# Optimization experiments

Hardware: AMD Instinct MI355X
Metric: run time of the kernel (lower is better)

## Reference

```python
import jax, jax.numpy as jnp
import numpy as np

N, B, D, Q = 32, 36, 2048, 1024  # batch, objects, v_dim, q_dim


def setup_inputs() -> dict:
    key = jax.random.key(0)
    ks = jax.random.split(key, 6)
    sc = 0.02  # small init so ReLU chains stay well-scaled
    return {
        "v": jax.random.normal(ks[0], (N, B, D), jnp.float32),
        "q": jax.random.normal(ks[1], (N, Q), jnp.float32),
        "W1": jax.random.normal(ks[2], (D, D), jnp.float32) * sc,
        "b1": jnp.zeros((D,), jnp.float32),
        "W2": jax.random.normal(ks[3], (D, D), jnp.float32) * sc,
        "b2": jnp.zeros((D,), jnp.float32),
        "W3": jax.random.normal(ks[4], (Q, D), jnp.float32) * sc,
        "b3": jnp.zeros((D,), jnp.float32),
    }


def reference(v, q, W1, b1, W2, b2, W3, b3):
    # FCNet = ReLU(Linear(.)) with weight-norm folded, dropout=0 (eval).
    # Original calls linear3 twice (linear4 unused bug), so q_emb == q_emb2.
    qe = jax.nn.relu(q @ W3 + b3)  # (N, D)
    # pairs[n,i,j] = v[n,i]*qe[n] + v[n,j]*qe[n]  -> (N, B, B, D)
    pairs = (v[:, :, None, :] + v[:, None, :, :]) * qe[:, None, None, :]
    h = jax.nn.relu(jnp.einsum('nijd,de->nije', pairs, W1) + b1)  # linear1
    x = jnp.sum(h, axis=2)  # sum over j relations -> (N, B, D)
    return jax.nn.relu(x @ W2 + b2)  # linear2
```

## Files before the change

### kernel.cpp

```cpp
#include <hip/hip_runtime.h>
#include <stdint.h>

#define N_BATCH 32
#define B_OBJ   36
#define D_DIM   2048
#define Q_DIM   1024

typedef __bf16 bf16x8  __attribute__((ext_vector_type(8)));
typedef float  f32x4   __attribute__((ext_vector_type(4)));
typedef float  f32x16  __attribute__((ext_vector_type(16)));

__device__ __forceinline__ uint16_t f2bf(float f) {
    uint32_t u = __builtin_bit_cast(uint32_t, f);
    uint32_t r = (u + 0x7FFFu + ((u >> 16) & 1u)) >> 16;
    return (uint16_t)r;
}

__device__ __forceinline__ void gld_lds16(const void* g, void* l) {
    __builtin_amdgcn_global_load_lds(
        (const __attribute__((address_space(1))) uint32_t*)g,
        (__attribute__((address_space(3))) uint32_t*)l, 16, 0, 0);
}

__global__ __launch_bounds__(256) void transpose_all(
    const float* __restrict__ W1, const float* __restrict__ W2,
    uint16_t* __restrict__ W1t, uint16_t* __restrict__ W2t) {
    __shared__ float tile[64][65];
    int gy = blockIdx.y;
    const float* W; uint16_t* Wt; int k0;
    if (gy < 32) { W = W1; Wt = W1t; k0 = gy * 64; }
    else         { W = W2; Wt = W2t; k0 = (gy - 32) * 64; }
    int n0 = blockIdx.x * 64;
    int t = threadIdx.x;
    {
        int r = t >> 4, c = (t & 15) * 4;
#pragma unroll
        for (int p = 0; p < 4; ++p)
            *(float4*)&tile[r + p * 16][c] =
                *(const float4*)&W[(size_t)(k0 + r + p * 16) * 2048 + n0 + c];
    }
    __syncthreads();
    {
        int n = t >> 2, kb = (t & 3) * 16;
#pragma unroll
        for (int g4 = 0; g4 < 4; ++g4) {
            int k = kb + g4 * 4;
            ushort4 o;
            o.x = f2bf(tile[k][n]);     o.y = f2bf(tile[k + 1][n]);
            o.z = f2bf(tile[k + 2][n]); o.w = f2bf(tile[k + 3][n]);
            *(ushort4*)&Wt[(size_t)(n0 + n) * 2048 + k0 + k] = o;
        }
    }
}

__global__ __launch_bounds__(256) void qe_f32(
    const float* __restrict__ q, const float* __restrict__ W3,
    float* __restrict__ qpart) {
    __shared__ float qs[128][32];
    int t = threadIdx.x;
    int e0 = blockIdx.x * 64;
    int kbase = blockIdx.y * 128;
    {
        int nn = t >> 3, kg = (t & 7) * 16;
#pragma unroll
        for (int p = 0; p < 4; ++p) {
            float4 f = *(const float4*)&q[(size_t)nn * Q_DIM + kbase + kg + p * 4];
            qs[kg + p * 4 + 0][nn] = f.x; qs[kg + p * 4 + 1][nn] = f.y;
            qs[kg + p * 4 + 2][nn] = f.z; qs[kg + p * 4 + 3][nn] = f.w;
        }
    }
    __syncthreads();
    int n = t >> 3, e8 = (t & 7) * 8;
    float acc[8] = {};
#pragma unroll 4
    for (int k = 0; k < 128; ++k) {
        float qv = qs[k][n];
        float4 wa = *(const float4*)&W3[(size_t)(kbase + k) * D_DIM + e0 + e8];
        float4 wb = *(const float4*)&W3[(size_t)(kbase + k) * D_DIM + e0 + e8 + 4];
        acc[0] += qv * wa.x; acc[1] += qv * wa.y; acc[2] += qv * wa.z; acc[3] += qv * wa.w;
        acc[4] += qv * wb.x; acc[5] += qv * wb.y; acc[6] += qv * wb.z; acc[7] += qv * wb.w;
    }
    float* dst = qpart + (size_t)blockIdx.y * 32 * D_DIM + (size_t)n * D_DIM + e0 + e8;
    *(float4*)dst = *(float4*)&acc[0];
    *(float4*)(dst + 4) = *(float4*)&acc[4];
}

__global__ __launch_bounds__(256) void qe_makeu(
    const float* __restrict__ qpart, const float* __restrict__ b3,
    const float* __restrict__ v, uint16_t* __restrict__ u) {
    int n = blockIdx.y;
    int c4 = blockIdx.x * 256 + threadIdx.x;
    const float4* p = (const float4*)qpart;
    size_t base = (size_t)n * 512 + c4;
    float4 s = p[base];
#pragma unroll
    for (int z = 1; z < 8; ++z) {
        float4 sz = p[(size_t)z * 16384 + base];
        s.x += sz.x; s.y += sz.y; s.z += sz.z; s.w += sz.w;
    }
    float4 b = ((const float4*)b3)[c4];
    float4 qe;
    qe.x = fmaxf(s.x + b.x, 0.f); qe.y = fmaxf(s.y + b.y, 0.f);
    qe.z = fmaxf(s.z + b.z, 0.f); qe.w = fmaxf(s.w + b.w, 0.f);
    const float4* v4 = (const float4*)v + (size_t)n * B_OBJ * 512 + c4;
    ushort4* u4 = (ushort4*)u + (size_t)n * B_OBJ * 512 + c4;
#pragma unroll 4
    for (int i = 0; i < B_OBJ; ++i) {
        float4 vv = v4[(size_t)i * 512];
        ushort4 o;
        o.x = f2bf(vv.x * qe.x); o.y = f2bf(vv.y * qe.y);
        o.z = f2bf(vv.z * qe.z); o.w = f2bf(vv.w * qe.w);
        u4[(size_t)i * 512] = o;
    }
}

__global__ __launch_bounds__(128) void gemm_fused(
    const uint16_t* __restrict__ A,
    const uint16_t* __restrict__ Bt,
    const float* __restrict__ bias,
    void* __restrict__ Cv,
    int mode) {
    __shared__ __align__(16) uint16_t sm[20480];
    float* yt = (float*)sm;

    int t = threadIdx.x, lane = t & 63, wave = t >> 6;
    int l31 = lane & 31, khalf = lane >> 5;
    int bg = blockIdx.y;
    int n0 = blockIdx.x * 64;
    const uint16_t* Ab = A + (size_t)bg * 72 * D_DIM;

    const uint16_t* gp[10]; uint16_t* lp[10]; int bufstep[10];
    {
        int row16 = lane >> 2, kin = (lane & 3) * 8;
#pragma unroll
        for (int c = 0; c < 10; ++c) {
            int r = wave * 10 + c;
            if (r < 12) {
                int h = r / 6, g = r % 6;
                gp[c] = Ab + (size_t)(g * 16 + row16) * D_DIM + h * 32 + kin;
                lp[c] = sm + h * 3072 + g * 512;
                bufstep[c] = 6144;
            } else {
                int rb = r - 12, h = rb >> 2, g = rb & 3;
                gp[c] = Bt + (size_t)(n0 + g * 16 + row16) * D_DIM + h * 32 + kin;
                lp[c] = sm + 12288 + h * 2048 + g * 512;
                bufstep[c] = 4096;
            }
        }
    }

    f32x16 acc[3] = {};

#pragma unroll
    for (int c = 0; c < 10; ++c) gld_lds16(gp[c], lp[c]);

    for (int it = 0; it < 32; ++it) {
        int buf = it & 1;
        __syncthreads();
        if (it < 31) {
            int nxt = buf ^ 1;
#pragma unroll
            for (int c = 0; c < 10; ++c)
                gld_lds16(gp[c] + (size_t)(it + 1) * 64, lp[c] + nxt * bufstep[c]);
        }
#pragma unroll
        for (int s = 0; s < 4; ++s) {
            int h = s >> 1, kin = (s & 1) * 16 + khalf * 8;
            bf16x8 bfr = *(const bf16x8*)(sm + 12288 + buf * 4096 + h * 2048 +
                                          (wave * 32 + l31) * 32 + kin);
#pragma unroll
            for (int mt = 0; mt < 3; ++mt) {
                bf16x8 af = *(const bf16x8*)(sm + buf * 6144 + h * 3072 +
                                             (mt * 32 + l31) * 32 + kin);
                acc[mt] = __builtin_amdgcn_mfma_f32_32x32x16_bf16(af, bfr, acc[mt], 0, 0, 0);
            }
        }
    }

    if (mode == 0) {
        uint16_t* X = (uint16_t*)Cv;
        __syncthreads();
#pragma unroll
        for (int mt = 0; mt < 3; ++mt)
#pragma unroll
            for (int reg = 0; reg < 16; ++reg) {
                int row = mt * 32 + (reg & 3) + 8 * (reg >> 2) + 4 * khalf;
                if (row < 72) yt[row * 68 + wave * 32 + l31] = acc[mt][reg];
            }
        __syncthreads();
        int col = t & 63, half = t >> 6;
        float b = bias[n0 + col];
        float z[36];
#pragma unroll
        for (int j = 0; j < 36; ++j) z[j] = yt[(half * 36 + j) * 68 + col];
        uint16_t* xb = X + (size_t)(bg * 72 + half * 36) * D_DIM + n0 + col;
#pragma unroll
        for (int i = 0; i < 36; ++i) {
            float zi = z[i] + b;
            float ssum = 0.f;
#pragma unroll
            for (int j = 0; j < 36; ++j) ssum += fmaxf(zi + z[j], 0.f);
            xb[(size_t)i * D_DIM] = f2bf(ssum);
        }
    } else {
        float* O = (float*)Cv;
        int col = n0 + wave * 32 + l31;
        float b = bias[col];
#pragma unroll
        for (int mt = 0; mt < 3; ++mt)
#pragma unroll
            for (int reg = 0; reg < 16; ++reg) {
                int row = mt * 32 + (reg & 3) + 8 * (reg >> 2) + 4 * khalf;
                if (row < 72)
                    O[(size_t)(bg * 72 + row) * D_DIM + col] =
                        fmaxf(acc[mt][reg] + b, 0.f);
            }
    }
}

extern "C" void kernel_launch(void* const* d_in, const int* in_sizes, int n_in,
                              void* d_out, int out_size, void* d_ws, size_t ws_size,
                              hipStream_t stream) {
    const float* v  = (const float*)d_in[0];
    const float* q  = (const float*)d_in[1];
    const float* W1 = (const float*)d_in[2];
    const float* b1 = (const float*)d_in[3];
    const float* W2 = (const float*)d_in[4];
    const float* b2 = (const float*)d_in[5];
    const float* W3 = (const float*)d_in[6];
    const float* b3 = (const float*)d_in[7];
    float* out = (float*)d_out;

    char* ws = (char*)d_ws;
    uint16_t* W1t   = (uint16_t*)(ws + 0);
    uint16_t* W2t   = (uint16_t*)(ws + 8388608);
    uint16_t* u     = (uint16_t*)(ws + 16777216);
    float*    qpart = (float*)   (ws + 21495808);
    uint16_t* x     = (uint16_t*)(ws + 23592960);

    transpose_all<<<dim3(32, 64), 256, 0, stream>>>(W1, W2, W1t, W2t);

    qe_f32<<<dim3(32, 8), 256, 0, stream>>>(q, W3, qpart);
    qe_makeu<<<dim3(2, N_BATCH), 256, 0, stream>>>(qpart, b3, v, u);

    gemm_fused<<<dim3(32, 16), 128, 0, stream>>>(u, W1t, b1, x, 0);

    gemm_fused<<<dim3(32, 16), 128, 0, stream>>>(x, W2t, b2, out, 1);
}
```

Before: 190.3 us.

## Split fused GEMM into 64x64-tile GEMM plus separate pairwise-sum kernel

```diff
diff --git a/kernel.cpp b/kernel.cpp
--- a/kernel.cpp
+++ b/kernel.cpp
@@ -114,45 +114,48 @@
     }
 }
 
-__global__ __launch_bounds__(128) void gemm_fused(
+__global__ __launch_bounds__(256) void gemm64(
     const uint16_t* __restrict__ A,
     const uint16_t* __restrict__ Bt,
     const float* __restrict__ bias,
-    void* __restrict__ Cv,
+    float* __restrict__ C,
     int mode) {
-    __shared__ __align__(16) uint16_t sm[20480];
-    float* yt = (float*)sm;
+    __shared__ __align__(16) uint16_t sm[17408];
 
     int t = threadIdx.x, lane = t & 63, wave = t >> 6;
     int l31 = lane & 31, khalf = lane >> 5;
-    int bg = blockIdx.y;
-    int n0 = blockIdx.x * 64;
-    const uint16_t* Ab = A + (size_t)bg * 72 * D_DIM;
-
-    const uint16_t* gp[10]; uint16_t* lp[10]; int bufstep[10];
-    {
-        int row16 = lane >> 2, kin = (lane & 3) * 8;
-#pragma unroll
-        for (int c = 0; c < 10; ++c) {
-            int r = wave * 10 + c;
-            if (r < 12) {
-                int h = r / 6, g = r % 6;
-                gp[c] = Ab + (size_t)(g * 16 + row16) * D_DIM + h * 32 + kin;
-                lp[c] = sm + h * 3072 + g * 512;
-                bufstep[c] = 6144;
+    int mq = wave >> 1, nq = wave & 1;
+
+    int flat = blockIdx.y * 32 + blockIdx.x;
+    int n_t = (flat & 7) * 4 + ((flat >> 3) & 3);
+    int m_t = flat >> 5;
+    int m0 = m_t * 64, n0 = n_t * 64;
+
+    const uint16_t* Ab = A  + (size_t)m0 * D_DIM;
+    const uint16_t* Bb = Bt + (size_t)n0 * D_DIM;
+
+    const uint16_t* gp[4]; uint16_t* lp[4];
+    {
+        int ri = lane & 15, k8 = lane >> 4;
+#pragma unroll
+        for (int c = 0; c < 4; ++c) {
+            int r = wave * 4 + c;
+            if (r < 8) {
+                int h = r >> 2, g = r & 3;
+                gp[c] = Ab + (size_t)(g * 16 + ri) * D_DIM + h * 32 + k8 * 8;
+                lp[c] = sm + h * 2176 + g * 544;
             } else {
-                int rb = r - 12, h = rb >> 2, g = rb & 3;
-                gp[c] = Bt + (size_t)(n0 + g * 16 + row16) * D_DIM + h * 32 + kin;
-                lp[c] = sm + 12288 + h * 2048 + g * 512;
-                bufstep[c] = 4096;
+                int rb = r - 8, h = rb >> 2, g = rb & 3;
+                gp[c] = Bb + (size_t)(g * 16 + ri) * D_DIM + h * 32 + k8 * 8;
+                lp[c] = sm + 8704 + h * 2176 + g * 544;
             }
         }
     }
 
-    f32x16 acc[3] = {};
-
-#pragma unroll
-    for (int c = 0; c < 10; ++c) gld_lds16(gp[c], lp[c]);
+    f32x16 acc = {};
+
+#pragma unroll
+    for (int c = 0; c < 4; ++c) gld_lds16(gp[c], lp[c]);
 
     for (int it = 0; it < 32; ++it) {
         int buf = it & 1;
@@ -160,61 +163,51 @@
         if (it < 31) {
             int nxt = buf ^ 1;
 #pragma unroll
-            for (int c = 0; c < 10; ++c)
-                gld_lds16(gp[c] + (size_t)(it + 1) * 64, lp[c] + nxt * bufstep[c]);
-        }
+            for (int c = 0; c < 4; ++c)
+                gld_lds16(gp[c] + (size_t)(it + 1) * 64, lp[c] + nxt * 4352);
+        }
+        int gA = mq * 2 + (l31 >> 4), gB = nq * 2 + (l31 >> 4);
+        int ri8 = (l31 & 15) * 8;
 #pragma unroll
         for (int s = 0; s < 4; ++s) {
-            int h = s >> 1, kin = (s & 1) * 16 + khalf * 8;
-            bf16x8 bfr = *(const bf16x8*)(sm + 12288 + buf * 4096 + h * 2048 +
-                                          (wave * 32 + l31) * 32 + kin);
-#pragma unroll
-            for (int mt = 0; mt < 3; ++mt) {
-                bf16x8 af = *(const bf16x8*)(sm + buf * 6144 + h * 3072 +
-                                             (mt * 32 + l31) * 32 + kin);
-                acc[mt] = __builtin_amdgcn_mfma_f32_32x32x16_bf16(af, bfr, acc[mt], 0, 0, 0);
-            }
-        }
-    }
-
-    if (mode == 0) {
-        uint16_t* X = (uint16_t*)Cv;
-        __syncthreads();
-#pragma unroll
-        for (int mt = 0; mt < 3; ++mt)
-#pragma unroll
-            for (int reg = 0; reg < 16; ++reg) {
-                int row = mt * 32 + (reg & 3) + 8 * (reg >> 2) + 4 * khalf;
-                if (row < 72) yt[row * 68 + wave * 32 + l31] = acc[mt][reg];
-            }
-        __syncthreads();
-        int col = t & 63, half = t >> 6;
-        float b = bias[n0 + col];
-        float z[36];
-#pragma unroll
-        for (int j = 0; j < 36; ++j) z[j] = yt[(half * 36 + j) * 68 + col];
-        uint16_t* xb = X + (size_t)(bg * 72 + half * 36) * D_DIM + n0 + col;
-#pragma unroll
-        for (int i = 0; i < 36; ++i) {
-            float zi = z[i] + b;
-            float ssum = 0.f;
-#pragma unroll
-            for (int j = 0; j < 36; ++j) ssum += fmaxf(zi + z[j], 0.f);
-            xb[(size_t)i * D_DIM] = f2bf(ssum);
-        }
-    } else {
-        float* O = (float*)Cv;
-        int col = n0 + wave * 32 + l31;
-        float b = bias[col];
-#pragma unroll
-        for (int mt = 0; mt < 3; ++mt)
-#pragma unroll
-            for (int reg = 0; reg < 16; ++reg) {
-                int row = mt * 32 + (reg & 3) + 8 * (reg >> 2) + 4 * khalf;
-                if (row < 72)
-                    O[(size_t)(bg * 72 + row) * D_DIM + col] =
-                        fmaxf(acc[mt][reg] + b, 0.f);
-            }
+            int h = s >> 1, k8i = (s & 1) * 2 + khalf;
+            bf16x8 af = *(const bf16x8*)(sm + buf * 4352 + h * 2176 +
+                                         gA * 544 + k8i * 128 + ri8);
+            bf16x8 bfr = *(const bf16x8*)(sm + 8704 + buf * 4352 + h * 2176 +
+                                          gB * 544 + k8i * 128 + ri8);
+            acc = __builtin_amdgcn_mfma_f32_32x32x16_bf16(af, bfr, acc, 0, 0, 0);
+        }
+    }
+
+    int col = n0 + nq * 32 + l31;
+    float b = (mode == 1) ? bias[col] : 0.f;
+#pragma unroll
+    for (int reg = 0; reg < 16; ++reg) {
+        int row = m0 + mq * 32 + (reg & 3) + 8 * (reg >> 2) + 4 * khalf;
+        float val = acc[reg] + b;
+        if (mode == 1) val = fmaxf(val, 0.f);
+        C[(size_t)row * D_DIM + col] = val;
+    }
+}
+
+__global__ __launch_bounds__(256) void pairsum(
+    const float* __restrict__ y, const float* __restrict__ b1,
+    uint16_t* __restrict__ X) {
+    int n = blockIdx.y;
+    int d = blockIdx.x * 256 + threadIdx.x;
+    const float* yb = y + (size_t)(n * B_OBJ) * D_DIM + d;
+    float z[B_OBJ];
+#pragma unroll
+    for (int j = 0; j < B_OBJ; ++j) z[j] = yb[(size_t)j * D_DIM];
+    float b = b1[d];
+    uint16_t* xb = X + (size_t)(n * B_OBJ) * D_DIM + d;
+#pragma unroll
+    for (int i = 0; i < B_OBJ; ++i) {
+        float zi = z[i] + b;
+        float s = 0.f;
+#pragma unroll
+        for (int j = 0; j < B_OBJ; ++j) s += fmaxf(zi + z[j], 0.f);
+        xb[(size_t)i * D_DIM] = f2bf(s);
     }
 }
 
@@ -237,13 +230,16 @@
     uint16_t* u     = (uint16_t*)(ws + 16777216);
     float*    qpart = (float*)   (ws + 21495808);
     uint16_t* x     = (uint16_t*)(ws + 23592960);
+    float*    y     = (float*)   (ws + 28311552);
 
     transpose_all<<<dim3(32, 64), 256, 0, stream>>>(W1, W2, W1t, W2t);
 
     qe_f32<<<dim3(32, 8), 256, 0, stream>>>(q, W3, qpart);
     qe_makeu<<<dim3(2, N_BATCH), 256, 0, stream>>>(qpart, b3, v, u);
 
-    gemm_fused<<<dim3(32, 16), 128, 0, stream>>>(u, W1t, b1, x, 0);
-
-    gemm_fused<<<dim3(32, 16), 128, 0, stream>>>(x, W2t, b2, out, 1);
-}
+    gemm64<<<dim3(32, 18), 256, 0, stream>>>(u, W1t, nullptr, y, 0);
+
+    pairsum<<<dim3(8, N_BATCH), 256, 0, stream>>>(y, b1, x);
+
+    gemm64<<<dim3(32, 18), 256, 0, stream>>>(x, W2t, b2, out, 1);
+}
```

After: 224.1 us. 1.18x slower.
